# Performance work log

Measured on AMD Instinct MI355X. Metric: run time of the kernel, lower is better.

## Reference

```python
import jax, jax.numpy as jnp
import numpy as np

N, D, E, H, O, K = 4096, 1024, 8, 2048, 1024, 2
LOSS_COEF = 0.01


def setup_inputs() -> dict:
    key = jax.random.key(0)
    ks = jax.random.split(key, 8)
    x = jax.random.normal(ks[0], (N, D), jnp.float32)
    return {
        "x": x,
        "x_offsets": jnp.array([0, N // 2, N], jnp.int32),  # unused by forward math
        "max_seq_len": 2048,
        "group_norm": False,
        "num_groups": 8,
        "linear_dim": D // 8,
        "norm_weight": jax.random.uniform(ks[1], (D,), jnp.float32, 0.5, 1.5),
        "norm_bias": jax.random.normal(ks[2], (D,), jnp.float32) * 0.1,
        "norm_eps": 1e-5,
        "w_gate": jax.random.normal(ks[3], (D, E), jnp.float32) * (1.0 / np.sqrt(D)),
        "experts_hidden_w": jax.random.normal(ks[4], (E, H, D), jnp.float32) * 0.02,
        "experts_hidden_bias": jnp.zeros((E, H), jnp.float32),
        "experts_w": jax.random.normal(ks[5], (E, O, H), jnp.float32) * 0.02,
        "experts_bias": jnp.zeros((E, O), jnp.float32),
        "output_weight": jax.random.normal(ks[6], (D, O), jnp.float32) * 0.02,
    }


def _cv_squared(v, eps=1e-6):
    v = v.astype(jnp.float32)
    m = v.mean()
    return jnp.var(v, ddof=1) / (m * m + eps)  # torch .var() is unbiased


def reference(x, x_offsets, max_seq_len, group_norm, num_groups, linear_dim,
              norm_weight, norm_bias, norm_eps,
              w_gate, experts_hidden_w, experts_hidden_bias,
              experts_w, experts_bias, output_weight):
    # ---- input normalization (layer_norm branch; group_norm=False) ----
    if group_norm:
        xg = x.reshape(-1, num_groups, linear_dim)
        mu = xg.mean(axis=2, keepdims=True)
        var = ((xg - mu) ** 2).mean(axis=2, keepdims=True)
        xg = (xg - mu) * jax.lax.rsqrt(var + norm_eps)
        xg = xg * norm_weight[None, :, None] + norm_bias[None, :, None]
        x_norm = xg.reshape(-1, x.shape[-1])
    else:
        mu = x.mean(axis=-1, keepdims=True)
        var = ((x - mu) ** 2).mean(axis=-1, keepdims=True)  # biased, like F.layer_norm
        x_norm = (x - mu) * jax.lax.rsqrt(var + norm_eps) * norm_weight + norm_bias

    # ---- gating: clean logits (enable_noisy_gating=False), L2-normalize rows ----
    logits = x_norm @ w_gate                                  # [N, E]
    logits = logits / jnp.maximum(
        jnp.linalg.norm(logits, axis=1, keepdims=True), 1e-12)
    probs = jax.nn.softmax(logits, axis=1)                    # softmax over all experts
    _, top_idx = jax.lax.top_k(logits, K)                     # [N, K]
    gates_k = jnp.take_along_axis(probs, top_idx, axis=1)     # top-k of softmax(logits)
    rows = jnp.arange(logits.shape[0])[:, None]
    gates = jnp.zeros_like(logits).at[rows, top_idx].set(gates_k)  # [N, E] sparse gates

    # ---- load-balancing loss (train=True, non-noisy path) ----
    importance = gates.sum(axis=0)
    load = (gates > 0).sum(axis=0).astype(jnp.float32)
    loss = (_cv_squared(importance) + _cv_squared(load)) * LOSS_COEF

    # ---- expert MLPs; gates are exactly zero off top-k so masked-dense == dispatch ----
    h = jax.nn.silu(jnp.einsum('nd,ehd->enh', x_norm, experts_hidden_w)
                    + experts_hidden_bias[:, None, :])        # [E, N, H]
    eo = jnp.einsum('enh,eoh->eno', h, experts_w) + experts_bias[:, None, :]  # [E, N, O]
    y_moe = jnp.einsum('ne,eno->no', gates.astype(jnp.float32),
                       eo.astype(jnp.float32))                # fp32 combine, like index_add

    # ---- residual projection: addmm(y_moe, x, output_weight) ----
    y = y_moe + x @ output_weight
    gate_fraction = load / load.sum()
    return (y, loss, gate_fraction)
```

## Files before the change

kernel.cpp:

```cpp
#include <hip/hip_runtime.h>
#include <hip/hip_bf16.h>
#include <stdint.h>

#define N_TOK 4096
#define DIM   1024
#define NE    8
#define NH    2048
#define NO    1024

typedef __attribute__((ext_vector_type(8))) short bf16x8;
typedef __attribute__((ext_vector_type(16))) float f32x16;

__device__ inline unsigned short f2bf(float f) {
    unsigned u = __float_as_uint(f);
    u += 0x7fffu + ((u >> 16) & 1u);
    return (unsigned short)(u >> 16);
}

__device__ inline void async_copy16(const void* g, void* l) {
    __builtin_amdgcn_global_load_lds(
        (const __attribute__((address_space(1))) void*)g,
        (__attribute__((address_space(3))) void*)l, 16, 0, 0);
}

#define LN_BLK  4096
#define CVT_BLK 32768
__global__ __launch_bounds__(256) void fused_prep_kernel(
    const float* __restrict__ x, const float* __restrict__ nw,
    const float* __restrict__ nb, const float* __restrict__ eps_p,
    const float* __restrict__ wg,
    unsigned short* __restrict__ xn_bf, unsigned short* __restrict__ x_bf,
    int* __restrict__ tok_e, float* __restrict__ tok_g,
    const float* __restrict__ whw, unsigned short* __restrict__ wh_bf,
    const float* __restrict__ wow, unsigned short* __restrict__ wo_bf,
    const float* __restrict__ wout, unsigned short* __restrict__ wt_bf)
{
    __shared__ float tile[32][33];
    __shared__ float rs[4], rs2[4];
    __shared__ float gred[4][NE];

    int b = blockIdx.x, t = threadIdx.x;

    if (b < LN_BLK) {
        int n = b;
        int lane = t & 63, wv = t >> 6;

        const float4 xv = ((const float4*)(x + (size_t)n * DIM))[t];
        float s  = xv.x + xv.y + xv.z + xv.w;
        float s2 = xv.x*xv.x + xv.y*xv.y + xv.z*xv.z + xv.w*xv.w;
        #pragma unroll
        for (int o = 32; o > 0; o >>= 1) {
            s  += __shfl_down(s, o);
            s2 += __shfl_down(s2, o);
        }
        if (lane == 0) { rs[wv] = s; rs2[wv] = s2; }
        __syncthreads();
        float S  = rs[0] + rs[1] + rs[2] + rs[3];
        float S2 = rs2[0] + rs2[1] + rs2[2] + rs2[3];
        const float inv = 1.0f / (float)DIM;
        float mu = S * inv;
        float var = fmaxf(S2 * inv - mu * mu, 0.0f);
        float rstd = rsqrtf(var + eps_p[0]);

        float4 w4 = ((const float4*)nw)[t];
        float4 b4 = ((const float4*)nb)[t];
        float xn0 = (xv.x - mu) * rstd * w4.x + b4.x;
        float xn1 = (xv.y - mu) * rstd * w4.y + b4.y;
        float xn2 = (xv.z - mu) * rstd * w4.z + b4.z;
        float xn3 = (xv.w - mu) * rstd * w4.w + b4.w;

        ushort4 pn; pn.x = f2bf(xn0); pn.y = f2bf(xn1); pn.z = f2bf(xn2); pn.w = f2bf(xn3);
        ((ushort4*)(xn_bf + (size_t)n * DIM))[t] = pn;
        ushort4 px; px.x = f2bf(xv.x); px.y = f2bf(xv.y); px.z = f2bf(xv.z); px.w = f2bf(xv.w);
        ((ushort4*)(x_bf + (size_t)n * DIM))[t] = px;

        float acc[NE];
        #pragma unroll
        for (int e = 0; e < NE; ++e) acc[e] = 0.0f;
        float xns[4] = {xn0, xn1, xn2, xn3};
        const float4* wgp = (const float4*)(wg + (size_t)(4 * t) * NE);
        #pragma unroll
        for (int j = 0; j < 4; ++j) {
            float4 w0 = wgp[2 * j], w1 = wgp[2 * j + 1];
            float xj = xns[j];
            acc[0] += xj * w0.x; acc[1] += xj * w0.y; acc[2] += xj * w0.z; acc[3] += xj * w0.w;
            acc[4] += xj * w1.x; acc[5] += xj * w1.y; acc[6] += xj * w1.z; acc[7] += xj * w1.w;
        }
        #pragma unroll
        for (int o = 32; o > 0; o >>= 1) {
            #pragma unroll
            for (int e = 0; e < NE; ++e) acc[e] += __shfl_down(acc[e], o);
        }
        if (lane == 0) {
            #pragma unroll
            for (int e = 0; e < NE; ++e) gred[wv][e] = acc[e];
        }
        __syncthreads();
        if (t == 0) {
            float lg[NE];
            float nrm2 = 0.0f;
            #pragma unroll
            for (int e = 0; e < NE; ++e) {
                lg[e] = gred[0][e] + gred[1][e] + gred[2][e] + gred[3][e];
                nrm2 += lg[e] * lg[e];
            }
            float den = fmaxf(sqrtf(nrm2), 1e-12f);
            float linv = 1.0f / den;
            #pragma unroll
            for (int e = 0; e < NE; ++e) lg[e] *= linv;
            float mx = lg[0];
            #pragma unroll
            for (int e = 1; e < NE; ++e) mx = fmaxf(mx, lg[e]);
            float p[NE], ps = 0.0f;
            #pragma unroll
            for (int e = 0; e < NE; ++e) { p[e] = expf(lg[e] - mx); ps += p[e]; }
            float pinv = 1.0f / ps;
            #pragma unroll
            for (int e = 0; e < NE; ++e) p[e] *= pinv;
            int i0 = 0; float b0 = lg[0];
            #pragma unroll
            for (int e = 1; e < NE; ++e) if (lg[e] > b0) { b0 = lg[e]; i0 = e; }
            int i1 = -1; float b1 = -3.0e38f;
            #pragma unroll
            for (int e = 0; e < NE; ++e) if (e != i0 && lg[e] > b1) { b1 = lg[e]; i1 = e; }
            tok_e[2 * n] = i0; tok_e[2 * n + 1] = i1;
            tok_g[2 * n] = p[i0]; tok_g[2 * n + 1] = p[i1];
        }
        return;
    }

    int b2 = b - LN_BLK;
    if (b2 < CVT_BLK) {
        const int n4each = NE * NH * DIM / 4;
        int i = b2 * 256 + t;
        const float4* s; ushort4* d; int j;
        if (i < n4each) { s = (const float4*)whw; d = (ushort4*)wh_bf; j = i; }
        else            { s = (const float4*)wow; d = (ushort4*)wo_bf; j = i - n4each; }
        float4 v = s[j];
        ushort4 o; o.x = f2bf(v.x); o.y = f2bf(v.y); o.z = f2bf(v.z); o.w = f2bf(v.w);
        d[j] = o;
        return;
    }

    int idx = b2 - CVT_BLK;
    int o0 = (idx & 31) * 32, d0 = (idx >> 5) * 32;
    int tx = t & 31, ty0 = t >> 5;
    #pragma unroll
    for (int k = 0; k < 4; ++k) {
        int ty = ty0 + k * 8;
        tile[ty][tx] = wout[(size_t)(d0 + ty) * NO + o0 + tx];
    }
    __syncthreads();
    #pragma unroll
    for (int k = 0; k < 4; ++k) {
        int ty = ty0 + k * 8;
        wt_bf[(size_t)(o0 + ty) * DIM + d0 + tx] = f2bf(tile[tx][ty]);
    }
}

__device__ inline float cv_sq(const float* v) {
    float m = 0.0f;
    for (int e = 0; e < NE; ++e) m += v[e];
    m *= (1.0f / NE);
    float s = 0.0f;
    for (int e = 0; e < NE; ++e) { float d = v[e] - m; s += d * d; }
    s *= (1.0f / (NE - 1));
    return s / (m * m + 1e-6f);
}

__global__ __launch_bounds__(256) void routing_kernel(
    const int* __restrict__ tok_e, const float* __restrict__ tok_g,
    int* __restrict__ counts, int* __restrict__ offsets,
    int* __restrict__ rowsbuf, int* __restrict__ invslot,
    float* __restrict__ out_tail)
{
    __shared__ int   sc[4][NE], sp[4][NE];
    __shared__ float sf[4][NE];
    __shared__ int   lcur[NE];

    int rb = blockIdx.x, t = threadIdx.x;
    int lane = t & 63, wv = t >> 6;
    int chunk0 = rb * 1024;

    int lc[NE]; float li[NE];
    #pragma unroll
    for (int e = 0; e < NE; ++e) { lc[e] = 0; li[e] = 0.0f; }
    int base = t * 32;
    #pragma unroll
    for (int q = 0; q < 8; ++q) {
        int4 e4 = *(const int4*)(tok_e + base + q * 4);
        float4 g4 = *(const float4*)(tok_g + base + q * 4);
        lc[e4.x]++; li[e4.x] += g4.x;
        lc[e4.y]++; li[e4.y] += g4.y;
        lc[e4.z]++; li[e4.z] += g4.z;
        lc[e4.w]++; li[e4.w] += g4.w;
    }
    int prior_flag = (base + 32 <= chunk0) ? 1 : 0;
    int lp[NE];
    #pragma unroll
    for (int e = 0; e < NE; ++e) lp[e] = prior_flag ? lc[e] : 0;

    #pragma unroll
    for (int o = 32; o > 0; o >>= 1) {
        #pragma unroll
        for (int e = 0; e < NE; ++e) {
            lc[e] += __shfl_down(lc[e], o);
            lp[e] += __shfl_down(lp[e], o);
            li[e] += __shfl_down(li[e], o);
        }
    }
    if (lane == 0) {
        #pragma unroll
        for (int e = 0; e < NE; ++e) { sc[wv][e] = lc[e]; sp[wv][e] = lp[e]; sf[wv][e] = li[e]; }
    }
    __syncthreads();
    if (t == 0) {
        int cnt[NE], pri[NE]; float imp[NE];
        for (int e = 0; e < NE; ++e) {
            cnt[e] = sc[0][e] + sc[1][e] + sc[2][e] + sc[3][e];
            pri[e] = sp[0][e] + sp[1][e] + sp[2][e] + sp[3][e];
            imp[e] = sf[0][e] + sf[1][e] + sf[2][e] + sf[3][e];
        }
        int off = 0;
        for (int e = 0; e < NE; ++e) {
            lcur[e] = off + pri[e];
            if (rb == 0) { counts[e] = cnt[e]; offsets[e] = off; }
            off += cnt[e];
        }
        if (rb == 0) {
            float lcf[NE], lif[NE];
            for (int e = 0; e < NE; ++e) { lcf[e] = (float)cnt[e]; lif[e] = imp[e]; }
            float tot = (float)off;
            out_tail[0] = 0.01f * (cv_sq(lif) + cv_sq(lcf));
            for (int e = 0; e < NE; ++e) out_tail[1 + e] = lcf[e] / tot;
        }
    }
    __syncthreads();

    int g0 = chunk0 + 4 * t;
    int4 e4 = *(const int4*)(tok_e + g0);
    int s0 = atomicAdd(&lcur[e4.x], 1);
    int s1 = atomicAdd(&lcur[e4.y], 1);
    int s2 = atomicAdd(&lcur[e4.z], 1);
    int s3 = atomicAdd(&lcur[e4.w], 1);
    int tok0 = g0 >> 1;
    rowsbuf[s0] = tok0;     rowsbuf[s1] = tok0;
    rowsbuf[s2] = tok0 + 1; rowsbuf[s3] = tok0 + 1;
    invslot[g0]     = s0;   invslot[g0 + 1] = s1;
    invslot[g0 + 2] = s2;   invslot[g0 + 3] = s3;
}

#define BK 64

__global__ __launch_bounds__(256) void gemm1_kernel(
    const unsigned short* __restrict__ xn,
    const unsigned short* __restrict__ wh,
    const float* __restrict__ hb,
    const int* __restrict__ rowsbuf,
    const int* __restrict__ counts, const int* __restrict__ offsets,
    unsigned short* __restrict__ hbuf)
{
    int e = blockIdx.z;
    int count = counts[e];
    {
        int slice = blockIdx.y * 16 + blockIdx.x;
        int k = slice & 7, j = slice >> 3;
        int tn_ = (k & 3) * 4 + (j & 3);
        int tm_ = (k >> 2) * 4 + ((j >> 2) & 3) + (j >> 4) * 8;
        if (tm_ * 128 >= count) return;
        int off = offsets[e];
        int tm = tm_, tn = tn_;

        __shared__ alignas(16) short As[128 * BK];
        __shared__ alignas(16) short Bs[128 * BK];

        int t = threadIdx.x;
        int c = t & 7, rl = t >> 3;
        int csw = (c ^ (rl & 7)) * 8;
        const unsigned short* aptr[4];
        const unsigned short* bptr[4];
        #pragma unroll
        for (int p = 0; p < 4; ++p) {
            int mrow = tm * 128 + p * 32 + rl;
            int mc = mrow < count ? mrow : count - 1;
            int token = rowsbuf[off + mc];
            aptr[p] = xn + (size_t)token * DIM;
            bptr[p] = wh + ((size_t)e * NH + tn * 128 + p * 32 + rl) * DIM;
        }

        int lane = t & 63, wvi = t >> 6;
        int wm = (wvi & 1) * 64, wn = (wvi >> 1) * 64;
        int l31 = lane & 31, h = lane >> 5, sw = l31 & 7;

        f32x16 acc[2][2];
        #pragma unroll
        for (int i = 0; i < 2; ++i)
            #pragma unroll
            for (int j2 = 0; j2 < 2; ++j2) acc[i][j2] = (f32x16)(0.0f);

        for (int kt = 0; kt < DIM / BK; ++kt) {
            int kb = kt * BK + csw;
            #pragma unroll
            for (int p = 0; p < 4; ++p)
                async_copy16(aptr[p] + kb, (char*)As + p * 4096 + t * 16);
            #pragma unroll
            for (int p = 0; p < 4; ++p)
                async_copy16(bptr[p] + kb, (char*)Bs + p * 4096 + t * 16);
            __syncthreads();
            #pragma unroll
            for (int ks = 0; ks < 4; ++ks) {
                int ph = ((ks * 2 + h) ^ sw) * 8;
                bf16x8 af[2], bfr[2];
                #pragma unroll
                for (int i = 0; i < 2; ++i)
                    af[i] = *(const bf16x8*)&As[(wm + i * 32 + l31) * BK + ph];
                #pragma unroll
                for (int j2 = 0; j2 < 2; ++j2)
                    bfr[j2] = *(const bf16x8*)&Bs[(wn + j2 * 32 + l31) * BK + ph];
                #pragma unroll
                for (int i = 0; i < 2; ++i)
                    #pragma unroll
                    for (int j2 = 0; j2 < 2; ++j2)
                        acc[i][j2] = __builtin_amdgcn_mfma_f32_32x32x16_bf16(af[i], bfr[j2], acc[i][j2], 0, 0, 0);
            }
            __syncthreads();
        }

        #pragma unroll
        for (int i = 0; i < 2; ++i) {
            #pragma unroll
            for (int j2 = 0; j2 < 2; ++j2) {
                int col = tn * 128 + wn + j2 * 32 + l31;
                float bias = hb[e * NH + col];
                #pragma unroll
                for (int r = 0; r < 16; ++r) {
                    int row_d = (r & 3) + 8 * (r >> 2) + 4 * h;
                    int m = tm * 128 + wm + i * 32 + row_d;
                    if (m < count) {
                        float v = acc[i][j2][r] + bias;
                        v = v / (1.0f + __expf(-v));
                        hbuf[(size_t)(off + m) * NH + col] = f2bf(v);
                    }
                }
            }
        }
    }
}

__global__ __launch_bounds__(256) void gemm2_kernel(
    const unsigned short* __restrict__ hbuf,
    const unsigned short* __restrict__ wo,
    const float* __restrict__ ob,
    const int* __restrict__ counts, const int* __restrict__ offsets,
    float* __restrict__ eo)
{
    int e = blockIdx.z;
    int count = counts[e];
    int slice = blockIdx.y * 8 + blockIdx.x;
    int k = slice & 7, j = slice >> 3;
    int tn = (k & 3) * 2 + (j & 1);
    int tm = (k >> 2) * 4 + ((j >> 1) & 3) + (j >> 3) * 8;
    if (tm * 128 >= count) return;
    int off = offsets[e];

    __shared__ alignas(16) short As[128 * BK];
    __shared__ alignas(16) short Bs[128 * BK];

    int t = threadIdx.x;
    int c = t & 7, rl = t >> 3;
    int csw = (c ^ (rl & 7)) * 8;
    const unsigned short* aptr[4];
    const unsigned short* bptr[4];
    #pragma unroll
    for (int p = 0; p < 4; ++p) {
        int mrow = tm * 128 + p * 32 + rl;
        int mc = mrow < count ? mrow : count - 1;
        aptr[p] = hbuf + (size_t)(off + mc) * NH;
        bptr[p] = wo + ((size_t)e * NO + tn * 128 + p * 32 + rl) * NH;
    }

    int lane = t & 63, wvi = t >> 6;
    int wm = (wvi & 1) * 64, wn = (wvi >> 1) * 64;
    int l31 = lane & 31, h = lane >> 5, sw = l31 & 7;

    f32x16 acc[2][2];
    #pragma unroll
    for (int i = 0; i < 2; ++i)
        #pragma unroll
        for (int j2 = 0; j2 < 2; ++j2) acc[i][j2] = (f32x16)(0.0f);

    for (int kt = 0; kt < NH / BK; ++kt) {
        int kb = kt * BK + csw;
        #pragma unroll
        for (int p = 0; p < 4; ++p)
            async_copy16(aptr[p] + kb, (char*)As + p * 4096 + t * 16);
        #pragma unroll
        for (int p = 0; p < 4; ++p)
            async_copy16(bptr[p] + kb, (char*)Bs + p * 4096 + t * 16);
        __syncthreads();
        #pragma unroll
        for (int ks = 0; ks < 4; ++ks) {
            int ph = ((ks * 2 + h) ^ sw) * 8;
            bf16x8 af[2], bfr[2];
            #pragma unroll
            for (int i = 0; i < 2; ++i)
                af[i] = *(const bf16x8*)&As[(wm + i * 32 + l31) * BK + ph];
            #pragma unroll
            for (int j2 = 0; j2 < 2; ++j2)
                bfr[j2] = *(const bf16x8*)&Bs[(wn + j2 * 32 + l31) * BK + ph];
            #pragma unroll
            for (int i = 0; i < 2; ++i)
                #pragma unroll
                for (int j2 = 0; j2 < 2; ++j2)
                    acc[i][j2] = __builtin_amdgcn_mfma_f32_32x32x16_bf16(af[i], bfr[j2], acc[i][j2], 0, 0, 0);
        }
        __syncthreads();
    }

    #pragma unroll
    for (int i = 0; i < 2; ++i) {
        #pragma unroll
        for (int j2 = 0; j2 < 2; ++j2) {
            int col = tn * 128 + wn + j2 * 32 + l31;
            float bias = ob[e * NO + col];
            #pragma unroll
            for (int r = 0; r < 16; ++r) {
                int row_d = (r & 3) + 8 * (r >> 2) + 4 * h;
                int m = tm * 128 + wm + i * 32 + row_d;
                if (m < count)
                    eo[(size_t)(off + m) * NO + col] = acc[i][j2][r] + bias;
            }
        }
    }
}

__global__ __launch_bounds__(256) void gemm_res_kernel(
    const unsigned short* __restrict__ xb,
    const unsigned short* __restrict__ wt,
    const float* __restrict__ eo,
    const int* __restrict__ invslot,
    const float* __restrict__ tok_g,
    float* __restrict__ y)
{
    int slice = blockIdx.y * 8 + blockIdx.x;
    int k = slice & 7, j = slice >> 3;
    int tn = (k & 1) * 4 + (j & 3);
    int tm = (k >> 1) * 16 + (j >> 2);

    __shared__ alignas(16) short As[64 * BK];
    __shared__ alignas(16) short Bs[128 * BK];

    int t = threadIdx.x;
    int c = t & 7, rl = t >> 3;
    int csw = (c ^ (rl & 7)) * 8;
    const unsigned short* aptr[2];
    const unsigned short* bptr[4];
    #pragma unroll
    for (int p = 0; p < 2; ++p)
        aptr[p] = xb + (size_t)(tm * 64 + p * 32 + rl) * DIM;
    #pragma unroll
    for (int p = 0; p < 4; ++p)
        bptr[p] = wt + (size_t)(tn * 128 + p * 32 + rl) * DIM;

    int lane = t & 63, wvi = t >> 6;
    int wm = (wvi & 1) * 32, wn = (wvi >> 1) * 64;
    int l31 = lane & 31, h = lane >> 5, sw = l31 & 7;

    f32x16 acc[2];
    #pragma unroll
    for (int j2 = 0; j2 < 2; ++j2) acc[j2] = (f32x16)(0.0f);

    for (int kt = 0; kt < DIM / BK; ++kt) {
        int kb = kt * BK + csw;
        #pragma unroll
        for (int p = 0; p < 2; ++p)
            async_copy16(aptr[p] + kb, (char*)As + p * 4096 + t * 16);
        #pragma unroll
        for (int p = 0; p < 4; ++p)
            async_copy16(bptr[p] + kb, (char*)Bs + p * 4096 + t * 16);
        __syncthreads();
        #pragma unroll
        for (int ks = 0; ks < 4; ++ks) {
            int ph = ((ks * 2 + h) ^ sw) * 8;
            bf16x8 af, bfr[2];
            af = *(const bf16x8*)&As[(wm + l31) * BK + ph];
            #pragma unroll
            for (int j2 = 0; j2 < 2; ++j2)
                bfr[j2] = *(const bf16x8*)&Bs[(wn + j2 * 32 + l31) * BK + ph];
            #pragma unroll
            for (int j2 = 0; j2 < 2; ++j2)
                acc[j2] = __builtin_amdgcn_mfma_f32_32x32x16_bf16(af, bfr[j2], acc[j2], 0, 0, 0);
        }
        __syncthreads();
    }

    #pragma unroll
    for (int r = 0; r < 16; ++r) {
        int row_d = (r & 3) + 8 * (r >> 2) + 4 * h;
        int row = tm * 64 + wm + row_d;
        int s0 = invslot[2 * row], s1 = invslot[2 * row + 1];
        float g0 = tok_g[2 * row], g1 = tok_g[2 * row + 1];
        #pragma unroll
        for (int j2 = 0; j2 < 2; ++j2) {
            int col = tn * 128 + wn + j2 * 32 + l31;
            y[(size_t)row * NO + col] = acc[j2][r]
                + g0 * eo[(size_t)s0 * NO + col]
                + g1 * eo[(size_t)s1 * NO + col];
        }
    }
}

extern "C" void kernel_launch(void* const* d_in, const int* in_sizes, int n_in,
                              void* d_out, int out_size, void* d_ws, size_t ws_size,
                              hipStream_t stream) {
    const float* x    = (const float*)d_in[0];
    const float* nw   = (const float*)d_in[6];
    const float* nb   = (const float*)d_in[7];
    const float* eps  = (const float*)d_in[8];
    const float* wg   = (const float*)d_in[9];
    const float* whw  = (const float*)d_in[10];
    const float* whb  = (const float*)d_in[11];
    const float* wow  = (const float*)d_in[12];
    const float* wob  = (const float*)d_in[13];
    const float* wout = (const float*)d_in[14];

    char* ws = (char*)d_ws;
    unsigned short* xn_bf = (unsigned short*)(ws + 0);
    unsigned short* x_bf  = (unsigned short*)(ws + 8388608);
    unsigned short* wh_bf = (unsigned short*)(ws + 16777216);
    unsigned short* wo_bf = (unsigned short*)(ws + 50331648);
    unsigned short* wt_bf = (unsigned short*)(ws + 83886080);
    unsigned short* hbuf  = (unsigned short*)(ws + 85983232);
    float* eo = (float*)(ws + 16777216);
    char* meta = ws + 119537664;
    int*   counts     = (int*)(meta + 0);
    int*   offsets    = (int*)(meta + 128);
    int*   tok_e      = (int*)(meta + 2048);
    float* tok_g      = (float*)(meta + 2048 + 32768);
    int*   rowsbuf    = (int*)(meta + 2048 + 65536);
    int*   invslot    = (int*)(meta + 2048 + 98304);

    float* y = (float*)d_out;
    float* out_tail = y + (size_t)N_TOK * NO;

    fused_prep_kernel<<<LN_BLK + CVT_BLK + 1024, 256, 0, stream>>>(
        x, nw, nb, eps, wg, xn_bf, x_bf, tok_e, tok_g,
        whw, wh_bf, wow, wo_bf, wout, wt_bf);
    routing_kernel<<<8, 256, 0, stream>>>(
        tok_e, tok_g, counts, offsets, rowsbuf, invslot, out_tail);
    gemm1_kernel<<<dim3(NH / 128, N_TOK / 128, NE), 256, 0, stream>>>(
        xn_bf, wh_bf, whb, rowsbuf, counts, offsets, hbuf);
    gemm2_kernel<<<dim3(NO / 128, N_TOK / 128, NE), 256, 0, stream>>>(
        hbuf, wo_bf, wob, counts, offsets, eo);
    gemm_res_kernel<<<dim3(NO / 128, N_TOK / 64), 256, 0, stream>>>(
        x_bf, wt_bf, eo, invslot, tok_g, y);
}
```

Baseline: 362.0 us.

## Overlap expert-output weight conversion with gemm1 via idle-block work stealing

The bf16 conversion of the second expert weight matrix and the transposed output-weight conversion move out of the prep kernel. gemm1 blocks whose row tile exceeds an expert's token count, and would otherwise exit at once, now grab conversion chunks from a global atomic counter that the routing kernel resets. The first expert weight conversion stays in prep but uses fewer blocks, each handling multiple iterations with an LDS bounce so it can store 16-byte bf16x8 packets. The aim is to hide weight-conversion bandwidth behind gemm1 compute, at the cost of atomic contention and possibly uneven tail work in gemm1.

```diff
diff --git a/kernel.cpp b/kernel.cpp
--- a/kernel.cpp
+++ b/kernel.cpp
@@ -23,138 +23,133 @@
         (__attribute__((address_space(3))) void*)l, 16, 0, 0);
 }
 
+__device__ inline bf16x8 pack_bf8(float4 a, float4 b) {
+    bf16x8 o;
+    o[0] = (short)f2bf(a.x); o[1] = (short)f2bf(a.y);
+    o[2] = (short)f2bf(a.z); o[3] = (short)f2bf(a.w);
+    o[4] = (short)f2bf(b.x); o[5] = (short)f2bf(b.y);
+    o[6] = (short)f2bf(b.z); o[7] = (short)f2bf(b.w);
+    return o;
+}
+
 #define LN_BLK  4096
-#define CVT_BLK 32768
-__global__ __launch_bounds__(256) void fused_prep_kernel(
+#define WH_BLK  1024
+#define WH_IT   8
+__global__ __launch_bounds__(256) void prep_kernel(
     const float* __restrict__ x, const float* __restrict__ nw,
     const float* __restrict__ nb, const float* __restrict__ eps_p,
     const float* __restrict__ wg,
     unsigned short* __restrict__ xn_bf, unsigned short* __restrict__ x_bf,
     int* __restrict__ tok_e, float* __restrict__ tok_g,
-    const float* __restrict__ whw, unsigned short* __restrict__ wh_bf,
-    const float* __restrict__ wow, unsigned short* __restrict__ wo_bf,
-    const float* __restrict__ wout, unsigned short* __restrict__ wt_bf)
+    const float* __restrict__ whw, unsigned short* __restrict__ wh_bf)
 {
-    __shared__ float tile[32][33];
+    __shared__ float4 bounce[512];
     __shared__ float rs[4], rs2[4];
     __shared__ float gred[4][NE];
 
     int b = blockIdx.x, t = threadIdx.x;
 
-    if (b < LN_BLK) {
-        int n = b;
-        int lane = t & 63, wv = t >> 6;
-
-        const float4 xv = ((const float4*)(x + (size_t)n * DIM))[t];
-        float s  = xv.x + xv.y + xv.z + xv.w;
-        float s2 = xv.x*xv.x + xv.y*xv.y + xv.z*xv.z + xv.w*xv.w;
-        #pragma unroll
-        for (int o = 32; o > 0; o >>= 1) {
-            s  += __shfl_down(s, o);
-            s2 += __shfl_down(s2, o);
-        }
-        if (lane == 0) { rs[wv] = s; rs2[wv] = s2; }
-        __syncthreads();
-        float S  = rs[0] + rs[1] + rs[2] + rs[3];
-        float S2 = rs2[0] + rs2[1] + rs2[2] + rs2[3];
-        const float inv = 1.0f / (float)DIM;
-        float mu = S * inv;
-        float var = fmaxf(S2 * inv - mu * mu, 0.0f);
-        float rstd = rsqrtf(var + eps_p[0]);
-
-        float4 w4 = ((const float4*)nw)[t];
-        float4 b4 = ((const float4*)nb)[t];
-        float xn0 = (xv.x - mu) * rstd * w4.x + b4.x;
-        float xn1 = (xv.y - mu) * rstd * w4.y + b4.y;
-        float xn2 = (xv.z - mu) * rstd * w4.z + b4.z;
-        float xn3 = (xv.w - mu) * rstd * w4.w + b4.w;
-
-        ushort4 pn; pn.x = f2bf(xn0); pn.y = f2bf(xn1); pn.z = f2bf(xn2); pn.w = f2bf(xn3);
-        ((ushort4*)(xn_bf + (size_t)n * DIM))[t] = pn;
-        ushort4 px; px.x = f2bf(xv.x); px.y = f2bf(xv.y); px.z = f2bf(xv.z); px.w = f2bf(xv.w);
-        ((ushort4*)(x_bf + (size_t)n * DIM))[t] = px;
-
-        float acc[NE];
-        #pragma unroll
-        for (int e = 0; e < NE; ++e) acc[e] = 0.0f;
-        float xns[4] = {xn0, xn1, xn2, xn3};
-        const float4* wgp = (const float4*)(wg + (size_t)(4 * t) * NE);
-        #pragma unroll
-        for (int j = 0; j < 4; ++j) {
-            float4 w0 = wgp[2 * j], w1 = wgp[2 * j + 1];
-            float xj = xns[j];
-            acc[0] += xj * w0.x; acc[1] += xj * w0.y; acc[2] += xj * w0.z; acc[3] += xj * w0.w;
-            acc[4] += xj * w1.x; acc[5] += xj * w1.y; acc[6] += xj * w1.z; acc[7] += xj * w1.w;
-        }
-        #pragma unroll
-        for (int o = 32; o > 0; o >>= 1) {
-            #pragma unroll
-            for (int e = 0; e < NE; ++e) acc[e] += __shfl_down(acc[e], o);
-        }
-        if (lane == 0) {
-            #pragma unroll
-            for (int e = 0; e < NE; ++e) gred[wv][e] = acc[e];
-        }
-        __syncthreads();
-        if (t == 0) {
-            float lg[NE];
-            float nrm2 = 0.0f;
-            #pragma unroll
-            for (int e = 0; e < NE; ++e) {
-                lg[e] = gred[0][e] + gred[1][e] + gred[2][e] + gred[3][e];
-                nrm2 += lg[e] * lg[e];
-            }
-            float den = fmaxf(sqrtf(nrm2), 1e-12f);
-            float linv = 1.0f / den;
-            #pragma unroll
-            for (int e = 0; e < NE; ++e) lg[e] *= linv;
-            float mx = lg[0];
-            #pragma unroll
-            for (int e = 1; e < NE; ++e) mx = fmaxf(mx, lg[e]);
-            float p[NE], ps = 0.0f;
-            #pragma unroll
-            for (int e = 0; e < NE; ++e) { p[e] = expf(lg[e] - mx); ps += p[e]; }
-            float pinv = 1.0f / ps;
-            #pragma unroll
-            for (int e = 0; e < NE; ++e) p[e] *= pinv;
-            int i0 = 0; float b0 = lg[0];
-            #pragma unroll
-            for (int e = 1; e < NE; ++e) if (lg[e] > b0) { b0 = lg[e]; i0 = e; }
-            int i1 = -1; float b1 = -3.0e38f;
-            #pragma unroll
-            for (int e = 0; e < NE; ++e) if (e != i0 && lg[e] > b1) { b1 = lg[e]; i1 = e; }
-            tok_e[2 * n] = i0; tok_e[2 * n + 1] = i1;
-            tok_g[2 * n] = p[i0]; tok_g[2 * n + 1] = p[i1];
+    if (b >= LN_BLK) {
+        int cb = b - LN_BLK;
+        const float4* s = (const float4*)whw;
+        bf16x8* d = (bf16x8*)wh_bf;
+        #pragma unroll
+        for (int k = 0; k < WH_IT; ++k) {
+            int fb = (cb * WH_IT + k) * 512;
+            float4 v0 = s[fb + t];
+            float4 v1 = s[fb + 256 + t];
+            __syncthreads();
+            bounce[t] = v0; bounce[t + 256] = v1;
+            __syncthreads();
+            float4 a = bounce[2 * t], c = bounce[2 * t + 1];
+            d[(fb >> 1) + t] = pack_bf8(a, c);
         }
         return;
     }
 
-    int b2 = b - LN_BLK;
-    if (b2 < CVT_BLK) {
-        const int n4each = NE * NH * DIM / 4;
-        int i = b2 * 256 + t;
-        const float4* s; ushort4* d; int j;
-        if (i < n4each) { s = (const float4*)whw; d = (ushort4*)wh_bf; j = i; }
-        else            { s = (const float4*)wow; d = (ushort4*)wo_bf; j = i - n4each; }
-        float4 v = s[j];
-        ushort4 o; o.x = f2bf(v.x); o.y = f2bf(v.y); o.z = f2bf(v.z); o.w = f2bf(v.w);
-        d[j] = o;
-        return;
-    }
-
-    int idx = b2 - CVT_BLK;
-    int o0 = (idx & 31) * 32, d0 = (idx >> 5) * 32;
-    int tx = t & 31, ty0 = t >> 5;
-    #pragma unroll
-    for (int k = 0; k < 4; ++k) {
-        int ty = ty0 + k * 8;
-        tile[ty][tx] = wout[(size_t)(d0 + ty) * NO + o0 + tx];
-    }
+    int n = b;
+    int lane = t & 63, wv = t >> 6;
+
+    const float4 xv = ((const float4*)(x + (size_t)n * DIM))[t];
+    float s  = xv.x + xv.y + xv.z + xv.w;
+    float s2 = xv.x*xv.x + xv.y*xv.y + xv.z*xv.z + xv.w*xv.w;
+    #pragma unroll
+    for (int o = 32; o > 0; o >>= 1) {
+        s  += __shfl_down(s, o);
+        s2 += __shfl_down(s2, o);
+    }
+    if (lane == 0) { rs[wv] = s; rs2[wv] = s2; }
     __syncthreads();
-    #pragma unroll
-    for (int k = 0; k < 4; ++k) {
-        int ty = ty0 + k * 8;
-        wt_bf[(size_t)(o0 + ty) * DIM + d0 + tx] = f2bf(tile[tx][ty]);
+    float S  = rs[0] + rs[1] + rs[2] + rs[3];
+    float S2 = rs2[0] + rs2[1] + rs2[2] + rs2[3];
+    const float inv = 1.0f / (float)DIM;
+    float mu = S * inv;
+    float var = fmaxf(S2 * inv - mu * mu, 0.0f);
+    float rstd = rsqrtf(var + eps_p[0]);
+
+    float4 w4 = ((const float4*)nw)[t];
+    float4 b4 = ((const float4*)nb)[t];
+    float xn0 = (xv.x - mu) * rstd * w4.x + b4.x;
+    float xn1 = (xv.y - mu) * rstd * w4.y + b4.y;
+    float xn2 = (xv.z - mu) * rstd * w4.z + b4.z;
+    float xn3 = (xv.w - mu) * rstd * w4.w + b4.w;
+
+    ushort4 pn; pn.x = f2bf(xn0); pn.y = f2bf(xn1); pn.z = f2bf(xn2); pn.w = f2bf(xn3);
+    ((ushort4*)(xn_bf + (size_t)n * DIM))[t] = pn;
+    ushort4 px; px.x = f2bf(xv.x); px.y = f2bf(xv.y); px.z = f2bf(xv.z); px.w = f2bf(xv.w);
+    ((ushort4*)(x_bf + (size_t)n * DIM))[t] = px;
+
+    float acc[NE];
+    #pragma unroll
+    for (int e = 0; e < NE; ++e) acc[e] = 0.0f;
+    float xns[4] = {xn0, xn1, xn2, xn3};
+    const float4* wgp = (const float4*)(wg + (size_t)(4 * t) * NE);
+    #pragma unroll
+    for (int j = 0; j < 4; ++j) {
+        float4 w0 = wgp[2 * j], w1 = wgp[2 * j + 1];
+        float xj = xns[j];
+        acc[0] += xj * w0.x; acc[1] += xj * w0.y; acc[2] += xj * w0.z; acc[3] += xj * w0.w;
+        acc[4] += xj * w1.x; acc[5] += xj * w1.y; acc[6] += xj * w1.z; acc[7] += xj * w1.w;
+    }
+    #pragma unroll
+    for (int o = 32; o > 0; o >>= 1) {
+        #pragma unroll
+        for (int e = 0; e < NE; ++e) acc[e] += __shfl_down(acc[e], o);
+    }
+    if (lane == 0) {
+        #pragma unroll
+        for (int e = 0; e < NE; ++e) gred[wv][e] = acc[e];
+    }
+    __syncthreads();
+    if (t == 0) {
+        float lg[NE];
+        float nrm2 = 0.0f;
+        #pragma unroll
+        for (int e = 0; e < NE; ++e) {
+            lg[e] = gred[0][e] + gred[1][e] + gred[2][e] + gred[3][e];
+            nrm2 += lg[e] * lg[e];
+        }
+        float den = fmaxf(sqrtf(nrm2), 1e-12f);
+        float linv = 1.0f / den;
+        #pragma unroll
+        for (int e = 0; e < NE; ++e) lg[e] *= linv;
+        float mx = lg[0];
+        #pragma unroll
+        for (int e = 1; e < NE; ++e) mx = fmaxf(mx, lg[e]);
+        float p[NE], ps = 0.0f;
+        #pragma unroll
+        for (int e = 0; e < NE; ++e) { p[e] = expf(lg[e] - mx); ps += p[e]; }
+        float pinv = 1.0f / ps;
+        #pragma unroll
+        for (int e = 0; e < NE; ++e) p[e] *= pinv;
+        int i0 = 0; float b0 = lg[0];
+        #pragma unroll
+        for (int e = 1; e < NE; ++e) if (lg[e] > b0) { b0 = lg[e]; i0 = e; }
+        int i1 = -1; float b1 = -3.0e38f;
+        #pragma unroll
+        for (int e = 0; e < NE; ++e) if (e != i0 && lg[e] > b1) { b1 = lg[e]; i1 = e; }
+        tok_e[2 * n] = i0; tok_e[2 * n + 1] = i1;
+        tok_g[2 * n] = p[i0]; tok_g[2 * n + 1] = p[i1];
     }
 }
 
@@ -172,7 +167,7 @@
     const int* __restrict__ tok_e, const float* __restrict__ tok_g,
     int* __restrict__ counts, int* __restrict__ offsets,
     int* __restrict__ rowsbuf, int* __restrict__ invslot,
-    float* __restrict__ out_tail)
+    float* __restrict__ out_tail, int* __restrict__ cvt_ctr)
 {
     __shared__ int   sc[4][NE], sp[4][NE];
     __shared__ float sf[4][NE];
@@ -228,6 +223,7 @@
             off += cnt[e];
         }
         if (rb == 0) {
+            *cvt_ctr = 0;
             float lcf[NE], lif[NE];
             for (int e = 0; e < NE; ++e) { lcf[e] = (float)cnt[e]; lif[e] = imp[e]; }
             float tot = (float)off;
@@ -252,95 +248,137 @@
 
 #define BK 64
 
+#define WO_F4      (NE * NO * NH / 4)
+#define WO_CHUNK   2048
+#define WO_CHUNKS  (WO_F4 / WO_CHUNK)
+#define CVT_TOT    (WO_CHUNKS + 1024)
+
 __global__ __launch_bounds__(256) void gemm1_kernel(
     const unsigned short* __restrict__ xn,
     const unsigned short* __restrict__ wh,
     const float* __restrict__ hb,
     const int* __restrict__ rowsbuf,
     const int* __restrict__ counts, const int* __restrict__ offsets,
-    unsigned short* __restrict__ hbuf)
+    unsigned short* __restrict__ hbuf,
+    const float* __restrict__ wow, unsigned short* __restrict__ wo_bf,
+    const float* __restrict__ wout, unsigned short* __restrict__ wt_bf,
+    int* __restrict__ cvt_ctr)
 {
+    __shared__ alignas(16) short As[128 * BK];
+    __shared__ alignas(16) short Bs[128 * BK];
+    __shared__ int sch;
+
     int e = blockIdx.z;
     int count = counts[e];
-    {
-        int slice = blockIdx.y * 16 + blockIdx.x;
-        int k = slice & 7, j = slice >> 3;
-        int tn_ = (k & 3) * 4 + (j & 3);
-        int tm_ = (k >> 2) * 4 + ((j >> 2) & 3) + (j >> 4) * 8;
-        if (tm_ * 128 >= count) return;
-        int off = offsets[e];
-        int tm = tm_, tn = tn_;
-
-        __shared__ alignas(16) short As[128 * BK];
-        __shared__ alignas(16) short Bs[128 * BK];
-
-        int t = threadIdx.x;
-        int c = t & 7, rl = t >> 3;
-        int csw = (c ^ (rl & 7)) * 8;
-        const unsigned short* aptr[4];
-        const unsigned short* bptr[4];
-        #pragma unroll
-        for (int p = 0; p < 4; ++p) {
-            int mrow = tm * 128 + p * 32 + rl;
-            int mc = mrow < count ? mrow : count - 1;
-            int token = rowsbuf[off + mc];
-            aptr[p] = xn + (size_t)token * DIM;
-            bptr[p] = wh + ((size_t)e * NH + tn * 128 + p * 32 + rl) * DIM;
-        }
-
-        int lane = t & 63, wvi = t >> 6;
-        int wm = (wvi & 1) * 64, wn = (wvi >> 1) * 64;
-        int l31 = lane & 31, h = lane >> 5, sw = l31 & 7;
-
-        f32x16 acc[2][2];
-        #pragma unroll
-        for (int i = 0; i < 2; ++i)
-            #pragma unroll
-            for (int j2 = 0; j2 < 2; ++j2) acc[i][j2] = (f32x16)(0.0f);
-
-        for (int kt = 0; kt < DIM / BK; ++kt) {
-            int kb = kt * BK + csw;
-            #pragma unroll
-            for (int p = 0; p < 4; ++p)
-                async_copy16(aptr[p] + kb, (char*)As + p * 4096 + t * 16);
-            #pragma unroll
-            for (int p = 0; p < 4; ++p)
-                async_copy16(bptr[p] + kb, (char*)Bs + p * 4096 + t * 16);
+    int t = threadIdx.x;
+    int slice = blockIdx.y * 16 + blockIdx.x;
+    int k = slice & 7, j = slice >> 3;
+    int tn = (k & 3) * 4 + (j & 3);
+    int tm = (k >> 2) * 4 + ((j >> 2) & 3) + (j >> 4) * 8;
+
+    if (tm * 128 >= count) {
+        for (;;) {
+            if (t == 0) sch = atomicAdd(cvt_ctr, 1);
             __syncthreads();
-            #pragma unroll
-            for (int ks = 0; ks < 4; ++ks) {
-                int ph = ((ks * 2 + h) ^ sw) * 8;
-                bf16x8 af[2], bfr[2];
+            int ch = sch;
+            __syncthreads();
+            if (ch >= CVT_TOT) return;
+            if (ch < WO_CHUNKS) {
+                const float4* s = (const float4*)wow + (size_t)ch * WO_CHUNK;
+                ushort4* dst = (ushort4*)wo_bf + (size_t)ch * WO_CHUNK;
                 #pragma unroll
-                for (int i = 0; i < 2; ++i)
-                    af[i] = *(const bf16x8*)&As[(wm + i * 32 + l31) * BK + ph];
+                for (int q = 0; q < WO_CHUNK / 256; ++q) {
+                    float4 v = s[q * 256 + t];
+                    ushort4 o4; o4.x = f2bf(v.x); o4.y = f2bf(v.y);
+                    o4.z = f2bf(v.z); o4.w = f2bf(v.w);
+                    dst[q * 256 + t] = o4;
+                }
+            } else {
+                float* tile = (float*)As;
+                int idx = ch - WO_CHUNKS;
+                int o0 = (idx & 31) * 32, d0 = (idx >> 5) * 32;
+                int tx = t & 31, ty0 = t >> 5;
+                #pragma unroll
+                for (int q = 0; q < 4; ++q) {
+                    int ty = ty0 + q * 8;
+                    tile[ty * 33 + tx] = wout[(size_t)(d0 + ty) * NO + o0 + tx];
+                }
+                __syncthreads();
+                #pragma unroll
+                for (int q = 0; q < 4; ++q) {
+                    int ty = ty0 + q * 8;
+                    wt_bf[(size_t)(o0 + ty) * DIM + d0 + tx] = f2bf(tile[tx * 33 + ty]);
+                }
+            }
+        }
+    }
+
+    int off = offsets[e];
+    int c = t & 7, rl = t >> 3;
+    int csw = (c ^ (rl & 7)) * 8;
+    const unsigned short* aptr[4];
+    const unsigned short* bptr[4];
+    #pragma unroll
+    for (int p = 0; p < 4; ++p) {
+        int mrow = tm * 128 + p * 32 + rl;
+        int mc = mrow < count ? mrow : count - 1;
+        int token = rowsbuf[off + mc];
+        aptr[p] = xn + (size_t)token * DIM;
+        bptr[p] = wh + ((size_t)e * NH + tn * 128 + p * 32 + rl) * DIM;
+    }
+
+    int lane = t & 63, wvi = t >> 6;
+    int wm = (wvi & 1) * 64, wn = (wvi >> 1) * 64;
+    int l31 = lane & 31, h = lane >> 5, sw = l31 & 7;
+
+    f32x16 acc[2][2];
+    #pragma unroll
+    for (int i = 0; i < 2; ++i)
+        #pragma unroll
+        for (int j2 = 0; j2 < 2; ++j2) acc[i][j2] = (f32x16)(0.0f);
+
+    for (int kt = 0; kt < DIM / BK; ++kt) {
+        int kb = kt * BK + csw;
+        #pragma unroll
+        for (int p = 0; p < 4; ++p)
+            async_copy16(aptr[p] + kb, (char*)As + p * 4096 + t * 16);
+        #pragma unroll
+        for (int p = 0; p < 4; ++p)
+            async_copy16(bptr[p] + kb, (char*)Bs + p * 4096 + t * 16);
+        __syncthreads();
+        #pragma unroll
+        for (int ks = 0; ks < 4; ++ks) {
+            int ph = ((ks * 2 + h) ^ sw) * 8;
+            bf16x8 af[2], bfr[2];
+            #pragma unroll
+            for (int i = 0; i < 2; ++i)
+                af[i] = *(const bf16x8*)&As[(wm + i * 32 + l31) * BK + ph];
+            #pragma unroll
+            for (int j2 = 0; j2 < 2; ++j2)
+                bfr[j2] = *(const bf16x8*)&Bs[(wn + j2 * 32 + l31) * BK + ph];
+            #pragma unroll
+            for (int i = 0; i < 2; ++i)
                 #pragma unroll
                 for (int j2 = 0; j2 < 2; ++j2)
-                    bfr[j2] = *(const bf16x8*)&Bs[(wn + j2 * 32 + l31) * BK + ph];
-                #pragma unroll
-                for (int i = 0; i < 2; ++i)
-                    #pragma unroll
-                    for (int j2 = 0; j2 < 2; ++j2)
-                        acc[i][j2] = __builtin_amdgcn_mfma_f32_32x32x16_bf16(af[i], bfr[j2], acc[i][j2], 0, 0, 0);
-            }
-            __syncthreads();
-        }
-
-        #pragma unroll
-        for (int i = 0; i < 2; ++i) {
-            #pragma unroll
-            for (int j2 = 0; j2 < 2; ++j2) {
-                int col = tn * 128 + wn + j2 * 32 + l31;
-                float bias = hb[e * NH + col];
-                #pragma unroll
-                for (int r = 0; r < 16; ++r) {
-                    int row_d = (r & 3) + 8 * (r >> 2) + 4 * h;
-                    int m = tm * 128 + wm + i * 32 + row_d;
-                    if (m < count) {
-                        float v = acc[i][j2][r] + bias;
-                        v = v / (1.0f + __expf(-v));
-                        hbuf[(size_t)(off + m) * NH + col] = f2bf(v);
-                    }
+                    acc[i][j2] = __builtin_amdgcn_mfma_f32_32x32x16_bf16(af[i], bfr[j2], acc[i][j2], 0, 0, 0);
+        }
+        __syncthreads();
+    }
+
+    #pragma unroll
+    for (int i = 0; i < 2; ++i) {
+        #pragma unroll
+        for (int j2 = 0; j2 < 2; ++j2) {
+            int col = tn * 128 + wn + j2 * 32 + l31;
+            float bias = hb[e * NH + col];
+            #pragma unroll
+            for (int r = 0; r < 16; ++r) {
+                int row_d = (r & 3) + 8 * (r >> 2) + 4 * h;
+                int m = tm * 128 + wm + i * 32 + row_d;
+                if (m < count) {
+                    float v = acc[i][j2][r] + bias;
+                    v = v / (1.0f + __expf(-v));
+                    hbuf[(size_t)(off + m) * NH + col] = f2bf(v);
                 }
             }
         }
@@ -539,17 +577,18 @@
     float* tok_g      = (float*)(meta + 2048 + 32768);
     int*   rowsbuf    = (int*)(meta + 2048 + 65536);
     int*   invslot    = (int*)(meta + 2048 + 98304);
+    int*   cvt_ctr    = (int*)(meta + 2048 + 131072 + 32768);
 
     float* y = (float*)d_out;
     float* out_tail = y + (size_t)N_TOK * NO;
 
-    fused_prep_kernel<<<LN_BLK + CVT_BLK + 1024, 256, 0, stream>>>(
-        x, nw, nb, eps, wg, xn_bf, x_bf, tok_e, tok_g,
-        whw, wh_bf, wow, wo_bf, wout, wt_bf);
+    prep_kernel<<<LN_BLK + WH_BLK, 256, 0, stream>>>(
+        x, nw, nb, eps, wg, xn_bf, x_bf, tok_e, tok_g, whw, wh_bf);
     routing_kernel<<<8, 256, 0, stream>>>(
-        tok_e, tok_g, counts, offsets, rowsbuf, invslot, out_tail);
+        tok_e, tok_g, counts, offsets, rowsbuf, invslot, out_tail, cvt_ctr);
     gemm1_kernel<<<dim3(NH / 128, N_TOK / 128, NE), 256, 0, stream>>>(
-        xn_bf, wh_bf, whb, rowsbuf, counts, offsets, hbuf);
+        xn_bf, wh_bf, whb, rowsbuf, counts, offsets, hbuf,
+        wow, wo_bf, wout, wt_bf, cvt_ctr);
     gemm2_kernel<<<dim3(NO / 128, N_TOK / 128, NE), 256, 0, stream>>>(
         hbuf, wo_bf, wob, counts, offsets, eo);
     gemm_res_kernel<<<dim3(NO / 128, N_TOK / 64), 256, 0, stream>>>(
```

Result: slower. 381.8 us (+5.5%).
